# Kernel optimization log

Hardware: AMD Instinct MI355X
Metric: run time of the kernel (lower is better)

Reference implementation:

```python
import jax, jax.numpy as jnp
import numpy as np

T, D, N = 131072, 512, 8


def setup_inputs() -> dict:
    key = jax.random.key(0)
    k1, k2, k3, k4 = jax.random.split(key, 4)
    x = jax.random.normal(k1, (T, D), dtype=jnp.float32)
    branch_idx = jax.random.randint(k2, (T,), 0, N, dtype=jnp.int32)
    # module inits weight to identity and bias to zero; use random values
    # (scaled like a trained projection) for a meaningful correctness test
    weight = jax.random.normal(k3, (N, D, D), dtype=jnp.float32) * (1.0 / np.sqrt(D))
    bias = jax.random.normal(k4, (N, D), dtype=jnp.float32) * 0.02
    return {"x": x, "branch_idx": branch_idx, "weight": weight, "bias": bias}


def reference(x, branch_idx, weight, bias):
    # Math: out[t] = x[t] @ weight[branch_idx[t]] + bias[branch_idx[t]]
    # Instead of materializing the gathered (T, D, D) weight tensor (as the
    # naive torch code does), run one dense GEMM per branch and select the
    # rows belonging to that branch. Same result, far less HBM traffic.
    num_branches = weight.shape[0]
    out = jnp.take(bias, branch_idx, axis=0)  # (T, D) gathered bias
    for n in range(num_branches):  # small fixed loop over branches
        mask = (branch_idx == n)[:, None]  # (T, 1)
        out = out + jnp.where(mask, x @ weight[n], jnp.zeros((), x.dtype))
    return out
```

## Files before the change

### kernel.cpp

```cpp
#include <hip/hip_runtime.h>
#include <hip/hip_bf16.h>
#include <stdint.h>

#define T_TOK 131072
#define DIM   512
#define NBR   8
#define BM    64
#define BK    32
#define NKT   (DIM / BK)
#define GT    512
#define MT    288

typedef __attribute__((ext_vector_type(8))) __bf16 bf16x8;
typedef __attribute__((ext_vector_type(4))) float  f32x4;
typedef unsigned short ushort_t;

__device__ __forceinline__ unsigned short f2bf(float f) {
  union { float f; unsigned int u; } v; v.f = f;
  unsigned int r = v.u + 0x7fffu + ((v.u >> 16) & 1u);
  return (unsigned short)(r >> 16);
}


__global__ void k_init(int* counts) {
  if (threadIdx.x < NBR) counts[threadIdx.x] = 0;
}

__global__ __launch_bounds__(512) void k_bhist(const int* __restrict__ bidx,
                                               int* __restrict__ counts) {
  __shared__ int h[NBR];
  if (threadIdx.x < NBR) h[threadIdx.x] = 0;
  __syncthreads();
  int t = blockIdx.x * 512 + threadIdx.x;
  atomicAdd(&h[bidx[t]], 1);
  __syncthreads();
  if (threadIdx.x < NBR) atomicAdd(&counts[threadIdx.x], h[threadIdx.x]);
}

__global__ void k_off(const int* __restrict__ counts, int* __restrict__ offsets,
                      int* __restrict__ cursors) {
  if (threadIdx.x == 0) {
    int s = 0;
    for (int n = 0; n < NBR; ++n) { offsets[n] = s; cursors[n] = s; s += counts[n]; }
  }
}

__global__ __launch_bounds__(512) void k_scatter(const int* __restrict__ bidx,
                                                 int* __restrict__ cursors,
                                                 int* __restrict__ perm) {
  __shared__ int h[NBR], base[NBR];
  if (threadIdx.x < NBR) h[threadIdx.x] = 0;
  __syncthreads();
  int t = blockIdx.x * 512 + threadIdx.x;
  int b = bidx[t];
  int rank = atomicAdd(&h[b], 1);
  __syncthreads();
  if (threadIdx.x < NBR)
    base[threadIdx.x] = atomicAdd(&cursors[threadIdx.x], h[threadIdx.x]);
  __syncthreads();
  perm[base[b] + rank] = t;
}

__global__ __launch_bounds__(256) void k_wtrans(const float* __restrict__ W,
                                                ushort_t* __restrict__ Wt) {
  __shared__ float tile[BK][129];
  int blk = blockIdx.x;
  int b  = blk >> 6;
  int kt = (blk >> 2) & 15;
  int cb = blk & 3;
  int t = threadIdx.x;
  #pragma unroll
  for (int i = 0; i < 4; ++i) {
    int idx4 = i * 256 + t;
    int kr = idx4 >> 5;
    int c4 = idx4 & 31;
    const float* src = W + (((size_t)b * DIM + (size_t)(kt * BK + kr)) * DIM + cb * 128 + c4 * 4);
    float4 v = *(const float4*)src;
    tile[kr][c4 * 4 + 0] = v.x;
    tile[kr][c4 * 4 + 1] = v.y;
    tile[kr][c4 * 4 + 2] = v.z;
    tile[kr][c4 * 4 + 3] = v.w;
  }
  __syncthreads();
  int c  = t >> 1;
  int kh = t & 1;
  unsigned int p[8];
  #pragma unroll
  for (int i = 0; i < 8; ++i) {
    unsigned short lo = f2bf(tile[kh * 16 + i * 2 + 0][c]);
    unsigned short hi = f2bf(tile[kh * 16 + i * 2 + 1][c]);
    p[i] = (unsigned int)lo | ((unsigned int)hi << 16);
  }
  size_t obase = (((size_t)b * 16 + kt) * DIM + (size_t)(cb * 128 + c)) * BK + kh * 16;
  uint4 q0; q0.x = p[0]; q0.y = p[1]; q0.z = p[2]; q0.w = p[3];
  uint4 q1; q1.x = p[4]; q1.y = p[5]; q1.z = p[6]; q1.w = p[7];
  *(uint4*)&Wt[obase]     = q0;
  *(uint4*)&Wt[obase + 8] = q1;
}

__global__ __launch_bounds__(GT, 4)
void k_gemm(const float* __restrict__ x, const float* __restrict__ bias,
            const ushort_t* __restrict__ Wt,
            const int* __restrict__ counts, const int* __restrict__ offsets,
            const int* __restrict__ perm, float* __restrict__ out) {
  __shared__ __align__(16) ushort_t As[NKT * 4 * 64 * 8];
  __shared__ int rowIdx[BM];

  const int tid = threadIdx.x;
  const int l = tid & 63;
  const int w = tid >> 6;

  const int b  = blockIdx.x / MT;
  const int lt = blockIdx.x % MT;
  const int cnt = counts[b];
  const int row0 = lt * BM;
  if (row0 >= cnt) return;
  const int gstart = offsets[b];
  const int vrows = min(BM, cnt - row0);

  if (tid < BM) {
    int r = row0 + tid; if (r >= cnt) r = cnt - 1;
    rowIdx[tid] = perm[gstart + r];
  }
  __syncthreads();

  const int arow = tid >> 3;
  const int kq = tid & 7;
  const float* aptr = x + (size_t)rowIdx[arow] * DIM + kq * 4;
  const int wbase = (((arow >> 4) * 64) + (kq >> 1) * 16 + (arow & 15)) * 8 + (kq & 1) * 4;

  {
    float4 xa = *(const float4*)aptr;
    float4 xb = *(const float4*)(aptr + BK);
    #pragma unroll
    for (int i = 0; i < NKT; ++i) {
      float4 xn;
      if (i + 2 < NKT) xn = *(const float4*)(aptr + (i + 2) * BK);
      ushort4 a4;
      a4.x = f2bf(xa.x); a4.y = f2bf(xa.y); a4.z = f2bf(xa.z); a4.w = f2bf(xa.w);
      *(ushort4*)&As[i * 2048 + wbase] = a4;
      xa = xb; xb = xn;
    }
  }
  __syncthreads();

  const ushort_t* wtile = Wt + (size_t)b * (NKT * BK * DIM);
  int bBase[4];
  #pragma unroll
  for (int cf = 0; cf < 4; ++cf)
    bBase[cf] = (w * 64 + cf * 16 + (l & 15)) * BK + (l >> 4) * 8;

  f32x4 acc[4][4];
  #pragma unroll
  for (int rf = 0; rf < 4; ++rf)
    #pragma unroll
    for (int cf = 0; cf < 4; ++cf) acc[rf][cf] = (f32x4){0.f, 0.f, 0.f, 0.f};

  bf16x8 bq[4];
  #pragma unroll
  for (int cf = 0; cf < 4; ++cf) bq[cf] = *(const bf16x8*)(wtile + bBase[cf]);

  #pragma unroll
  for (int kt = 0; kt < NKT; ++kt) {
    bf16x8 bqn[4];
    if (kt + 1 < NKT) {
      const ushort_t* wtk = wtile + (kt + 1) * (BK * DIM);
      #pragma unroll
      for (int cf = 0; cf < 4; ++cf) bqn[cf] = *(const bf16x8*)(wtk + bBase[cf]);
    }
    bf16x8 af[4];
    #pragma unroll
    for (int rf = 0; rf < 4; ++rf)
      af[rf] = *(const bf16x8*)&As[(kt * 4 + rf) * 512 + l * 8];
    #pragma unroll
    for (int cf = 0; cf < 4; ++cf)
      #pragma unroll
      for (int rf = 0; rf < 4; ++rf)
        acc[rf][cf] = __builtin_amdgcn_mfma_f32_16x16x32_bf16(af[rf], bq[cf], acc[rf][cf], 0, 0, 0);
    if (kt + 1 < NKT) {
      #pragma unroll
      for (int cf = 0; cf < 4; ++cf) bq[cf] = bqn[cf];
    }
  }

  float bv[4];
  #pragma unroll
  for (int cf = 0; cf < 4; ++cf) bv[cf] = bias[b * DIM + w * 64 + cf * 16 + (l & 15)];
  const int rb = (l >> 4) * 4;
  #pragma unroll
  for (int rf = 0; rf < 4; ++rf) {
    #pragma unroll
    for (int j = 0; j < 4; ++j) {
      int r = rf * 16 + rb + j;
      if (r < vrows) {
        float* op = out + (size_t)rowIdx[r] * DIM + w * 64 + (l & 15);
        #pragma unroll
        for (int cf = 0; cf < 4; ++cf) op[cf * 16] = acc[rf][cf][j] + bv[cf];
      }
    }
  }
}

extern "C" void kernel_launch(void* const* d_in, const int* in_sizes, int n_in,
                              void* d_out, int out_size, void* d_ws, size_t ws_size,
                              hipStream_t stream) {
  const float* x    = (const float*)d_in[0];
  const int*   bidx = (const int*)d_in[1];
  const float* W    = (const float*)d_in[2];
  const float* bias = (const float*)d_in[3];
  float* out = (float*)d_out;

  char* ws = (char*)d_ws;
  int* counts  = (int*)(ws + 0);
  int* cursors = (int*)(ws + 64);
  int* offsets = (int*)(ws + 128);
  int* perm    = (int*)(ws + 256);
  ushort_t* Wt = (ushort_t*)(ws + (1u << 20));

  k_init<<<1, 64, 0, stream>>>(counts);
  k_bhist<<<T_TOK / 512, 512, 0, stream>>>(bidx, counts);
  k_off<<<1, 64, 0, stream>>>(counts, offsets, cursors);
  k_scatter<<<T_TOK / 512, 512, 0, stream>>>(bidx, cursors, perm);
  k_wtrans<<<512, 256, 0, stream>>>(W, Wt);
  k_gemm<<<NBR * MT, GT, 0, stream>>>(x, bias, Wt, counts, offsets, perm, out);
}
```

Before: 205.8 us.

## Replace global histogram/scatter/GEMM pipeline with per-block local branch sort fused GEMM

Removes the four global histogram, offset and scatter kernels. Each 128-row block now counts and sorts its own rows by branch in shared memory, splits them into 16-row slices per branch, and runs MFMA against each slice's branch weights. Input rows are read contiguously and staged as bf16 in a swizzled shared-memory layout, with x loads overlapped with compute. The cost is padding waste on partial slices, repeated weight fetches per block for up to eight branches, and a possible second pass when a block has more than eight slices.

```diff
diff --git a/kernel.cpp b/kernel.cpp
--- a/kernel.cpp
+++ b/kernel.cpp
@@ -5,11 +5,12 @@
 #define T_TOK 131072
 #define DIM   512
 #define NBR   8
-#define BM    64
+#define ROWS  128
+#define NBLK  (T_TOK / ROWS)
 #define BK    32
 #define NKT   (DIM / BK)
-#define GT    512
-#define MT    288
+#define PLANE_U 4672
+#define MAXSL 16
 
 typedef __attribute__((ext_vector_type(8))) __bf16 bf16x8;
 typedef __attribute__((ext_vector_type(4))) float  f32x4;
@@ -19,46 +20,6 @@
   union { float f; unsigned int u; } v; v.f = f;
   unsigned int r = v.u + 0x7fffu + ((v.u >> 16) & 1u);
   return (unsigned short)(r >> 16);
-}
-
-
-__global__ void k_init(int* counts) {
-  if (threadIdx.x < NBR) counts[threadIdx.x] = 0;
-}
-
-__global__ __launch_bounds__(512) void k_bhist(const int* __restrict__ bidx,
-                                               int* __restrict__ counts) {
-  __shared__ int h[NBR];
-  if (threadIdx.x < NBR) h[threadIdx.x] = 0;
-  __syncthreads();
-  int t = blockIdx.x * 512 + threadIdx.x;
-  atomicAdd(&h[bidx[t]], 1);
-  __syncthreads();
-  if (threadIdx.x < NBR) atomicAdd(&counts[threadIdx.x], h[threadIdx.x]);
-}
-
-__global__ void k_off(const int* __restrict__ counts, int* __restrict__ offsets,
-                      int* __restrict__ cursors) {
-  if (threadIdx.x == 0) {
-    int s = 0;
-    for (int n = 0; n < NBR; ++n) { offsets[n] = s; cursors[n] = s; s += counts[n]; }
-  }
-}
-
-__global__ __launch_bounds__(512) void k_scatter(const int* __restrict__ bidx,
-                                                 int* __restrict__ cursors,
-                                                 int* __restrict__ perm) {
-  __shared__ int h[NBR], base[NBR];
-  if (threadIdx.x < NBR) h[threadIdx.x] = 0;
-  __syncthreads();
-  int t = blockIdx.x * 512 + threadIdx.x;
-  int b = bidx[t];
-  int rank = atomicAdd(&h[b], 1);
-  __syncthreads();
-  if (threadIdx.x < NBR)
-    base[threadIdx.x] = atomicAdd(&cursors[threadIdx.x], h[threadIdx.x]);
-  __syncthreads();
-  perm[base[b] + rank] = t;
 }
 
 __global__ __launch_bounds__(256) void k_wtrans(const float* __restrict__ W,
@@ -98,106 +59,167 @@
   *(uint4*)&Wt[obase + 8] = q1;
 }
 
-__global__ __launch_bounds__(GT, 4)
-void k_gemm(const float* __restrict__ x, const float* __restrict__ bias,
-            const ushort_t* __restrict__ Wt,
-            const int* __restrict__ counts, const int* __restrict__ offsets,
-            const int* __restrict__ perm, float* __restrict__ out) {
-  __shared__ __align__(16) ushort_t As[NKT * 4 * 64 * 8];
-  __shared__ int rowIdx[BM];
-
-  const int tid = threadIdx.x;
-  const int l = tid & 63;
-  const int w = tid >> 6;
-
-  const int b  = blockIdx.x / MT;
-  const int lt = blockIdx.x % MT;
-  const int cnt = counts[b];
-  const int row0 = lt * BM;
-  if (row0 >= cnt) return;
-  const int gstart = offsets[b];
-  const int vrows = min(BM, cnt - row0);
-
-  if (tid < BM) {
-    int r = row0 + tid; if (r >= cnt) r = cnt - 1;
-    rowIdx[tid] = perm[gstart + r];
-  }
-  __syncthreads();
-
-  const int arow = tid >> 3;
-  const int kq = tid & 7;
-  const float* aptr = x + (size_t)rowIdx[arow] * DIM + kq * 4;
-  const int wbase = (((arow >> 4) * 64) + (kq >> 1) * 16 + (arow & 15)) * 8 + (kq & 1) * 4;
-
-  {
-    float4 xa = *(const float4*)aptr;
-    float4 xb = *(const float4*)(aptr + BK);
-    #pragma unroll
-    for (int i = 0; i < NKT; ++i) {
-      float4 xn;
-      if (i + 2 < NKT) xn = *(const float4*)(aptr + (i + 2) * BK);
+__global__ __launch_bounds__(512, 2)
+void k_fused(const float* __restrict__ x, const int* __restrict__ bidx,
+             const ushort_t* __restrict__ Wt, const float* __restrict__ bias,
+             float* __restrict__ out) {
+  __shared__ ushort_t AT[NKT * PLANE_U];
+  __shared__ int cnt[NBR], pref[NBR];
+  __shared__ int sliceBaseL[MAXSL], sliceBrL[MAXSL], slimL[MAXSL];
+  __shared__ short slotOfL[ROWS];
+  __shared__ short pmapL[ROWS + 16];
+  __shared__ int tsL;
+
+  const int t  = threadIdx.x;
+  const int l  = t & 63;
+  const int li = l & 15;
+  const int c2 = l >> 4;
+  const int wv = t >> 6;
+  const int sgi = wv >> 2;
+  const int cg  = wv & 3;
+  const int row0 = blockIdx.x * ROWS;
+
+  if (t < NBR) cnt[t] = 0;
+  __syncthreads();
+  int myb = 0, myrank = 0;
+  if (t < ROWS) {
+    myb = bidx[row0 + t];
+    myrank = atomicAdd(&cnt[myb], 1);
+  }
+  __syncthreads();
+  if (t == 0) {
+    int s = 0, ns = 0;
+    for (int b = 0; b < NBR; ++b) {
+      pref[b] = s;
+      int c = cnt[b];
+      for (int o = 0; o < c; o += 16) {
+        sliceBaseL[ns] = s + o; sliceBrL[ns] = b; slimL[ns] = s + c; ++ns;
+      }
+      s += c;
+    }
+    tsL = ns;
+  }
+  __syncthreads();
+  if (t < ROWS) {
+    int slot = pref[myb] + myrank;
+    slotOfL[t] = (short)slot;
+    pmapL[slot] = (short)t;
+  }
+  __syncthreads();
+  const int nslice = tsL;
+
+  const int boff0 = ((cg << 7) + li) * BK + c2 * 8;
+  const float4* xp4 = (const float4*)(x + (size_t)row0 * DIM);
+
+  bool slv[4]; int sbrR[4], slimR[4], sbaseR[4], abase[4];
+  f32x4 acc[4][8];
+
+  auto load_slices = [&](int p) {
+    #pragma unroll
+    for (int s = 0; s < 4; ++s) {
+      int sl = p * 8 + sgi * 4 + s;
+      bool v = sl < nslice;
+      slv[s] = v;
+      int sb = v ? sliceBaseL[sl] : 0;
+      sbrR[s] = v ? sliceBrL[sl] : 0;
+      slimR[s] = v ? slimL[sl] : 0;
+      sbaseR[s] = sb;
+      int slot = sb + li;
+      int chp = (c2 | ((slot & 1) << 2)) ^ ((slot >> 1) & 7);
+      abase[s] = ((slot >> 1) << 6) + (chp << 3);
+    }
+  };
+  auto zero_acc = [&]() {
+    #pragma unroll
+    for (int s = 0; s < 4; ++s)
+      #pragma unroll
+      for (int cf = 0; cf < 8; ++cf) acc[s][cf] = (f32x4){0.f, 0.f, 0.f, 0.f};
+  };
+  auto computeKT = [&](int kt) {
+    int curbr = -1;
+    bf16x8 bq[8];
+    #pragma unroll
+    for (int s = 0; s < 4; ++s) {
+      if (slv[s]) {
+        if (sbrR[s] != curbr) {
+          curbr = sbrR[s];
+          const ushort_t* wp = Wt + ((size_t)(curbr * NKT + kt) << 14);
+          #pragma unroll
+          for (int cf = 0; cf < 8; ++cf) bq[cf] = *(const bf16x8*)(wp + boff0 + cf * 512);
+        }
+        bf16x8 af = *(const bf16x8*)&AT[abase[s] + kt * PLANE_U + ((kt & 7) << 3)];
+        #pragma unroll
+        for (int cf = 0; cf < 8; ++cf)
+          acc[s][cf] = __builtin_amdgcn_mfma_f32_16x16x32_bf16(af, bq[cf], acc[s][cf], 0, 0, 0);
+      }
+    }
+  };
+  auto epilogue = [&]() {
+    #pragma unroll
+    for (int s = 0; s < 4; ++s) {
+      if (!slv[s]) continue;
+      const int br = sbrR[s];
+      float bv[8];
+      #pragma unroll
+      for (int cf = 0; cf < 8; ++cf)
+        bv[cf] = bias[br * DIM + (cg << 7) + cf * 16 + li];
+      #pragma unroll
+      for (int j = 0; j < 4; ++j) {
+        int slot = sbaseR[s] + c2 * 4 + j;
+        if (slot < slimR[s]) {
+          int row = pmapL[slot];
+          float* op = out + ((size_t)(row0 + row)) * DIM + (cg << 7) + li;
+          #pragma unroll
+          for (int cf = 0; cf < 8; ++cf) op[cf * 16] = acc[s][cf][j] + bv[cf];
+        }
+      }
+    }
+  };
+
+  float4 v[8];
+  auto loadq = [&](int q) {
+    const float4* base = xp4 + q * 32;
+    #pragma unroll
+    for (int i = 0; i < 8; ++i) {
+      int row = i * 16 + (t >> 5);
+      int c = t & 31;
+      v[i] = base[row * 128 + c];
+    }
+  };
+  auto writeq = [&](int q) {
+    #pragma unroll
+    for (int i = 0; i < 8; ++i) {
+      int row = i * 16 + (t >> 5);
+      int c = t & 31;
+      int slot = slotOfL[row];
+      int kt = q * 4 + (c >> 3);
+      int chunk = (c >> 1) & 3;
+      int half = c & 1;
+      int chp = (chunk | ((slot & 1) << 2)) ^ ((slot >> 1) & 7);
+      int off = kt * PLANE_U + ((kt & 7) << 3) + ((slot >> 1) << 6) + (chp << 3) + (half << 2);
       ushort4 a4;
-      a4.x = f2bf(xa.x); a4.y = f2bf(xa.y); a4.z = f2bf(xa.z); a4.w = f2bf(xa.w);
-      *(ushort4*)&As[i * 2048 + wbase] = a4;
-      xa = xb; xb = xn;
-    }
-  }
-  __syncthreads();
-
-  const ushort_t* wtile = Wt + (size_t)b * (NKT * BK * DIM);
-  int bBase[4];
-  #pragma unroll
-  for (int cf = 0; cf < 4; ++cf)
-    bBase[cf] = (w * 64 + cf * 16 + (l & 15)) * BK + (l >> 4) * 8;
-
-  f32x4 acc[4][4];
-  #pragma unroll
-  for (int rf = 0; rf < 4; ++rf)
-    #pragma unroll
-    for (int cf = 0; cf < 4; ++cf) acc[rf][cf] = (f32x4){0.f, 0.f, 0.f, 0.f};
-
-  bf16x8 bq[4];
-  #pragma unroll
-  for (int cf = 0; cf < 4; ++cf) bq[cf] = *(const bf16x8*)(wtile + bBase[cf]);
-
-  #pragma unroll
-  for (int kt = 0; kt < NKT; ++kt) {
-    bf16x8 bqn[4];
-    if (kt + 1 < NKT) {
-      const ushort_t* wtk = wtile + (kt + 1) * (BK * DIM);
-      #pragma unroll
-      for (int cf = 0; cf < 4; ++cf) bqn[cf] = *(const bf16x8*)(wtk + bBase[cf]);
-    }
-    bf16x8 af[4];
-    #pragma unroll
-    for (int rf = 0; rf < 4; ++rf)
-      af[rf] = *(const bf16x8*)&As[(kt * 4 + rf) * 512 + l * 8];
-    #pragma unroll
-    for (int cf = 0; cf < 4; ++cf)
-      #pragma unroll
-      for (int rf = 0; rf < 4; ++rf)
-        acc[rf][cf] = __builtin_amdgcn_mfma_f32_16x16x32_bf16(af[rf], bq[cf], acc[rf][cf], 0, 0, 0);
-    if (kt + 1 < NKT) {
-      #pragma unroll
-      for (int cf = 0; cf < 4; ++cf) bq[cf] = bqn[cf];
-    }
-  }
-
-  float bv[4];
-  #pragma unroll
-  for (int cf = 0; cf < 4; ++cf) bv[cf] = bias[b * DIM + w * 64 + cf * 16 + (l & 15)];
-  const int rb = (l >> 4) * 4;
-  #pragma unroll
-  for (int rf = 0; rf < 4; ++rf) {
-    #pragma unroll
-    for (int j = 0; j < 4; ++j) {
-      int r = rf * 16 + rb + j;
-      if (r < vrows) {
-        float* op = out + (size_t)rowIdx[r] * DIM + w * 64 + (l & 15);
-        #pragma unroll
-        for (int cf = 0; cf < 4; ++cf) op[cf * 16] = acc[rf][cf][j] + bv[cf];
-      }
-    }
+      a4.x = f2bf(v[i].x); a4.y = f2bf(v[i].y); a4.z = f2bf(v[i].z); a4.w = f2bf(v[i].w);
+      *(ushort4*)&AT[off] = a4;
+    }
+  };
+
+  load_slices(0);
+  zero_acc();
+  loadq(0); writeq(0);
+  __syncthreads();
+  for (int q = 0; q < 4; ++q) {
+    if (q < 3) loadq(q + 1);
+    #pragma unroll
+    for (int k2 = 0; k2 < 4; ++k2) computeKT(q * 4 + k2);
+    if (q < 3) { writeq(q + 1); __syncthreads(); }
+  }
+  epilogue();
+
+  if (nslice > 8) {
+    load_slices(1);
+    zero_acc();
+    for (int kt = 0; kt < NKT; ++kt) computeKT(kt);
+    epilogue();
   }
 }
 
@@ -210,17 +232,8 @@
   const float* bias = (const float*)d_in[3];
   float* out = (float*)d_out;
 
-  char* ws = (char*)d_ws;
-  int* counts  = (int*)(ws + 0);
-  int* cursors = (int*)(ws + 64);
-  int* offsets = (int*)(ws + 128);
-  int* perm    = (int*)(ws + 256);
-  ushort_t* Wt = (ushort_t*)(ws + (1u << 20));
-
-  k_init<<<1, 64, 0, stream>>>(counts);
-  k_bhist<<<T_TOK / 512, 512, 0, stream>>>(bidx, counts);
-  k_off<<<1, 64, 0, stream>>>(counts, offsets, cursors);
-  k_scatter<<<T_TOK / 512, 512, 0, stream>>>(bidx, cursors, perm);
+  ushort_t* Wt = (ushort_t*)d_ws;
+
   k_wtrans<<<512, 256, 0, stream>>>(W, Wt);
-  k_gemm<<<NBR * MT, GT, 0, stream>>>(x, bias, Wt, counts, offsets, perm, out);
-}
+  k_fused<<<NBLK, 512, 0, stream>>>(x, bidx, Wt, bias, out);
+}
```

Measured after the change: 365.6 us. 1.78x slower.
